# Kernel tuning notes

Measured on AMD Instinct MI355X. Metric: run time of the kernel, lower is better.

## Reference

```python
import jax, jax.numpy as jnp
import numpy as np

N, E, F, K, T = 100000, 1600000, 64, 3, 2
EPS = 1e-5


def gcn_norm(row, col, edge_weight, num_nodes):
    # symmetric normalization WITHOUT self loops (PyG ARMAConv behavior)
    deg = jax.ops.segment_sum(edge_weight, col, num_segments=num_nodes)
    dis = jnp.where(deg > 0, jax.lax.rsqrt(deg), 0.0)
    return dis[row] * edge_weight * dis[col]


def arma_conv(x, row, col, norm, init_w, w, root_w, bias, num_nodes):
    # x: [N, Fin]; init_w: [K, Fin, Fout]; w: [K, T-1, Fout, Fout]
    # root_w: [K, T, Fin, Fout]; bias: [K, T, 1, Fout]
    n_layers = root_w.shape[1]
    out = jnp.einsum('nf,kfo->kno', x, init_w)  # [K, N, Fout]
    for t in range(n_layers):
        if t > 0:
            out = jnp.einsum('kno,kop->knp', out, w[:, t - 1])
        msg = out[:, row, :] * norm[None, :, None]  # [K, E, Fout]
        out = jax.vmap(lambda m: jax.ops.segment_sum(m, col, num_segments=num_nodes))(msg)
        out = out + jnp.einsum('nf,kfo->kno', x, root_w[:, t]) + bias[:, t]
        out = jax.nn.relu(out)  # ARMAConv act between layers and at output
    return out.mean(axis=0)  # mean over stacks -> [N, Fout]


def batchnorm(h, gamma, beta):
    mu = h.mean(axis=0)
    var = h.var(axis=0)
    return gamma * (h - mu) * jax.lax.rsqrt(var + EPS) + beta


def setup_inputs() -> dict:
    key = jax.random.key(0)
    ks = jax.random.split(key, 16)
    inp = {}
    inp['x'] = jax.random.normal(ks[0], (N, F), jnp.float32)
    inp['edge_index'] = jax.random.randint(ks[1], (2, E), 0, N, dtype=jnp.int32)
    inp['weights'] = jax.random.uniform(ks[2], (E,), jnp.float32)
    s = 0.1
    i = 3
    for c in (1, 2, 3):
        inp[f'iw{c}'] = jax.random.normal(ks[i], (K, F, F), jnp.float32) * s; i += 1
        inp[f'w{c}'] = jax.random.normal(ks[i], (K, T - 1, F, F), jnp.float32) * s; i += 1
        inp[f'rw{c}'] = jax.random.normal(ks[i], (K, T, F, F), jnp.float32) * s; i += 1
        inp[f'b{c}'] = jnp.zeros((K, T, 1, F), jnp.float32)
        inp[f'g{c}'] = jnp.ones((F,), jnp.float32)
        inp[f'be{c}'] = jnp.zeros((F,), jnp.float32)
    return inp


def reference(x, edge_index, weights,
              iw1, w1, rw1, b1, g1, be1,
              iw2, w2, rw2, b2, g2, be2,
              iw3, w3, rw3, b3, g3, be3):
    num_nodes = x.shape[0]
    row, col = edge_index[0], edge_index[1]
    norm = gcn_norm(row, col, weights, num_nodes)
    h = arma_conv(x, row, col, norm, iw1, w1, rw1, b1, num_nodes)
    h = jax.nn.relu(batchnorm(h, g1, be1))
    h = arma_conv(h, row, col, norm, iw2, w2, rw2, b2, num_nodes)
    h = jax.nn.relu(batchnorm(h, g2, be2))
    h = arma_conv(h, row, col, norm, iw3, w3, rw3, b3, num_nodes)
    h = jax.nn.relu(batchnorm(h, g3, be3))
    return h
```

## Files before the change

### kernel.cpp

```cpp
#include <hip/hip_runtime.h>

#define NN 100000
#define NE 1600000
#define FD 64
#define KK 3
#define NF (NN*FD)
#define EPSBN 1e-5f
#define SBLK ((NN + 255) / 256)
#define DEGSCALE 262144.0f

typedef unsigned short ushort;
typedef unsigned int uint;
typedef __attribute__((ext_vector_type(8))) short short8;
typedef __attribute__((ext_vector_type(4))) float f32x4;

__device__ inline float bf2f(ushort u) { return __uint_as_float((unsigned)u << 16); }
__device__ inline unsigned pk_bf16(float a, float b) {
  unsigned ua = __float_as_uint(a); ua += 0x7FFF + ((ua >> 16) & 1);
  unsigned ub = __float_as_uint(b); ub += 0x7FFF + ((ub >> 16) & 1);
  return (ua >> 16) | (ub & 0xFFFF0000u);
}
__device__ inline ushort f2bf(float v) {
  unsigned u = __float_as_uint(v); u += 0x7FFF + ((u >> 16) & 1);
  return (ushort)(u >> 16);
}

__global__ void k_degcnt(const int* __restrict__ col, const float* __restrict__ w,
                         unsigned long long* __restrict__ dc) {
  int e = blockIdx.x * 256 + threadIdx.x;
  if (e < NE) {
    unsigned fx = __float2uint_rn(w[e] * DEGSCALE);
    atomicAdd(&dc[col[e]], (1ULL << 32) | (unsigned long long)fx);
  }
}

__global__ __launch_bounds__(256) void k_sblk(const unsigned long long* __restrict__ dc,
                                              float* __restrict__ dis, int* __restrict__ cnt,
                                              int* __restrict__ part) {
  int i = blockIdx.x * 256 + threadIdx.x;
  int v = 0;
  if (i < NN) {
    unsigned long long u = dc[i];
    float d = (float)(unsigned)u * (1.0f / DEGSCALE);
    dis[i] = d > 0.f ? rsqrtf(d) : 0.f;
    v = (int)(u >> 32);
    cnt[i] = v;
  }
#pragma unroll
  for (int off = 32; off; off >>= 1) v += __shfl_down(v, off);
  __shared__ int ws[4];
  if ((threadIdx.x & 63) == 0) ws[threadIdx.x >> 6] = v;
  __syncthreads();
  if (threadIdx.x == 0) part[blockIdx.x] = ws[0] + ws[1] + ws[2] + ws[3];
}

__global__ __launch_bounds__(512) void k_sscan(const int* __restrict__ part,
                                               int* __restrict__ base) {
  __shared__ int ls[512];
  int tid = threadIdx.x;
  int v = (tid < SBLK) ? part[tid] : 0;
  ls[tid] = v;
  __syncthreads();
  for (int off = 1; off < 512; off <<= 1) {
    int u = (tid >= off) ? ls[tid - off] : 0;
    __syncthreads();
    ls[tid] += u;
    __syncthreads();
  }
  base[tid] = tid ? ls[tid - 1] : 0;
}

__global__ __launch_bounds__(256) void k_sfin(const int* __restrict__ cnt,
                                              const int* __restrict__ base,
                                              int* __restrict__ rowstart,
                                              int* __restrict__ cursor) {
  __shared__ int ls[256];
  int i = blockIdx.x * 256 + threadIdx.x;
  int v = (i < NN) ? cnt[i] : 0;
  ls[threadIdx.x] = v;
  __syncthreads();
  for (int off = 1; off < 256; off <<= 1) {
    int u = (threadIdx.x >= off) ? ls[threadIdx.x - off] : 0;
    __syncthreads();
    ls[threadIdx.x] += u;
    __syncthreads();
  }
  int excl = base[blockIdx.x] + ls[threadIdx.x] - v;
  if (i < NN) {
    rowstart[i] = excl;
    cursor[i] = excl;
    if (i == NN - 1) rowstart[NN] = excl + v;
  }
}

__global__ void k_place(const int* __restrict__ row, const int* __restrict__ col,
                        const float* __restrict__ w, const float* __restrict__ dis,
                        int* __restrict__ cursor, int2* __restrict__ edges) {
  int e = blockIdx.x * 256 + threadIdx.x;
  if (e >= NE) return;
  int r = row[e], c = col[e];
  float nm = dis[r] * w[e] * dis[c];
  int p = atomicAdd(&cursor[c], 1);
  edges[p] = make_int2(r, __float_as_int(nm));
}

__global__ __launch_bounds__(64) void k_wfrag(const float* __restrict__ iw,
                                              const float* __restrict__ w,
                                              const float* __restrict__ rw,
                                              uint4* __restrict__ frag) {
  int m = blockIdx.x;
  int which = m / 3, k = m % 3;
  const float* src;
  if (which == 0) src = iw + k * 4096;
  else if (which == 1) src = w + k * 4096;
  else if (which == 2) src = rw + k * 8192;
  else src = rw + k * 8192 + 4096;
  int sub = blockIdx.y;
  int ks = sub & 1, ct = sub >> 1;
  int l = threadIdx.x;
  int r0 = ks * 32 + (l >> 4) * 8;
  int c = ct * 16 + (l & 15);
  uint4 o;
  o.x = pk_bf16(src[(r0 + 0) * 64 + c], src[(r0 + 1) * 64 + c]);
  o.y = pk_bf16(src[(r0 + 2) * 64 + c], src[(r0 + 3) * 64 + c]);
  o.z = pk_bf16(src[(r0 + 4) * 64 + c], src[(r0 + 5) * 64 + c]);
  o.w = pk_bf16(src[(r0 + 6) * 64 + c], src[(r0 + 7) * 64 + c]);
  frag[(m * 8 + sub) * 64 + l] = o;
}

__global__ void k_tobf(const float* __restrict__ in, ushort* __restrict__ out) {
  long i = ((long)blockIdx.x * 256 + threadIdx.x) * 4;
  float4 v = *(const float4*)(in + i);
  uint2 u;
  u.x = pk_bf16(v.x, v.y);
  u.y = pk_bf16(v.z, v.w);
  *(uint2*)(out + i) = u;
}

#define RED2(v) do { (v) += __shfl_xor((v), 16); (v) += __shfl_xor((v), 32); } while (0)

#define G0STEP(EV) do { \
  int2 _e = (EV); \
  float _m = __int_as_float(_e.y); \
  uint2 _u = ((const uint2*)(xsrc + (long)_e.x * 64))[fi]; \
  a0 = fmaf(bf2f((ushort)_u.x), _m, a0); a1 = fmaf(bf2f((ushort)(_u.x >> 16)), _m, a1); \
  a2 = fmaf(bf2f((ushort)_u.y), _m, a2); a3 = fmaf(bf2f((ushort)(_u.y >> 16)), _m, a3); \
} while (0)

__global__ __launch_bounds__(256) void k_gath0(const int* __restrict__ rowstart,
                                               const int2* __restrict__ edges,
                                               const ushort* __restrict__ xsrc,
                                               ushort* __restrict__ g) {
  int wave = threadIdx.x >> 6;
  int lane = threadIdx.x & 63;
  int grp = lane >> 4;
  int fi = lane & 15;
  int n = blockIdx.x * 4 + wave;
  if (n >= NN) return;
  int s = rowstart[n], e = rowstart[n + 1];
  float a0 = 0.f, a1 = 0.f, a2 = 0.f, a3 = 0.f;
  int j = s;
  for (; j + 8 <= e; j += 8) {
    G0STEP(edges[j + grp]);
    G0STEP(edges[j + 4 + grp]);
  }
  if (j + 4 <= e) { G0STEP(edges[j + grp]); j += 4; }
  if (j < e) {
    int idx = j + grp;
    int2 ee = edges[idx < e ? idx : (e - 1)];
    if (idx >= e) ee.y = 0;
    G0STEP(ee);
  }
  RED2(a0); RED2(a1); RED2(a2); RED2(a3);
  if (grp == 0) {
    uint2 o;
    o.x = pk_bf16(a0, a1);
    o.y = pk_bf16(a2, a3);
    *(uint2*)(g + (long)n * 64 + 4 * fi) = o;
  }
}

#define G1STEP(EV) do { \
  int2 _e = (EV); \
  float _m = __int_as_float(_e.y); \
  const uint2* _p = (const uint2*)(y0 + (long)_e.x * 192) + fi; \
  uint2 _u0 = _p[0], _u1 = _p[16], _u2 = _p[32]; \
  a00 = fmaf(bf2f((ushort)_u0.x), _m, a00); a01 = fmaf(bf2f((ushort)(_u0.x >> 16)), _m, a01); \
  a02 = fmaf(bf2f((ushort)_u0.y), _m, a02); a03 = fmaf(bf2f((ushort)(_u0.y >> 16)), _m, a03); \
  a10 = fmaf(bf2f((ushort)_u1.x), _m, a10); a11 = fmaf(bf2f((ushort)(_u1.x >> 16)), _m, a11); \
  a12 = fmaf(bf2f((ushort)_u1.y), _m, a12); a13 = fmaf(bf2f((ushort)(_u1.y >> 16)), _m, a13); \
  a20 = fmaf(bf2f((ushort)_u2.x), _m, a20); a21 = fmaf(bf2f((ushort)(_u2.x >> 16)), _m, a21); \
  a22 = fmaf(bf2f((ushort)_u2.y), _m, a22); a23 = fmaf(bf2f((ushort)(_u2.y >> 16)), _m, a23); \
} while (0)

__global__ __launch_bounds__(256) void k_gath1(const int* __restrict__ rowstart,
                                               const int2* __restrict__ edges,
                                               const ushort* __restrict__ y0,
                                               ushort* __restrict__ G) {
  int wave = threadIdx.x >> 6;
  int lane = threadIdx.x & 63;
  int grp = lane >> 4;
  int fi = lane & 15;
  int n = blockIdx.x * 4 + wave;
  if (n >= NN) return;
  int s = rowstart[n], e = rowstart[n + 1];
  float a00 = 0.f, a01 = 0.f, a02 = 0.f, a03 = 0.f;
  float a10 = 0.f, a11 = 0.f, a12 = 0.f, a13 = 0.f;
  float a20 = 0.f, a21 = 0.f, a22 = 0.f, a23 = 0.f;
  int j = s;
  for (; j + 8 <= e; j += 8) {
    G1STEP(edges[j + grp]);
    G1STEP(edges[j + 4 + grp]);
  }
  if (j + 4 <= e) { G1STEP(edges[j + grp]); j += 4; }
  if (j < e) {
    int idx = j + grp;
    int2 ee = edges[idx < e ? idx : (e - 1)];
    if (idx >= e) ee.y = 0;
    G1STEP(ee);
  }
  RED2(a00); RED2(a01); RED2(a02); RED2(a03);
  RED2(a10); RED2(a11); RED2(a12); RED2(a13);
  RED2(a20); RED2(a21); RED2(a22); RED2(a23);
  if (grp < 3) {
    float aX, aY, aZ, aW;
    if (grp == 0)      { aX = a00; aY = a01; aZ = a02; aW = a03; }
    else if (grp == 1) { aX = a10; aY = a11; aZ = a12; aW = a13; }
    else               { aX = a20; aY = a21; aZ = a22; aW = a23; }
    uint2 o;
    o.x = pk_bf16(aX, aY);
    o.y = pk_bf16(aZ, aW);
    *(uint2*)(G + (long)n * 192 + grp * 64 + 4 * fi) = o;
  }
}

__global__ __launch_bounds__(256) void k_gemmY0(
    const ushort* __restrict__ g, const ushort* __restrict__ xbf,
    const uint4* __restrict__ wfA, const uint4* __restrict__ wfB,
    const float* __restrict__ bias, ushort* __restrict__ y0) {
  const int k = blockIdx.y;
  const int wv = threadIdx.x >> 6;
  const int l = threadIdx.x & 63;
  const int lg = l >> 4;
  const int lr = l & 15;
  short8 fA[4][2], fB[4][2];
#pragma unroll
  for (int ct = 0; ct < 4; ++ct)
#pragma unroll
    for (int ks = 0; ks < 2; ++ks) {
      fA[ct][ks] = *(const short8*)&wfA[(k * 8 + ct * 2 + ks) * 64 + l];
      fB[ct][ks] = *(const short8*)&wfB[(k * 8 + ct * 2 + ks) * 64 + l];
    }
  const int bb = blockIdx.x * 256;
  for (int rt = 0; rt < 4; ++rt) {
    const int tb = bb + rt * 64 + wv * 16;
    int ra = tb + lr; if (ra >= NN) ra = NN - 1;
    const long ao = (long)ra * 64 + lg * 8;
    short8 a0 = *(const short8*)(g + ao);
    short8 a1 = *(const short8*)(g + ao + 32);
    short8 b0 = *(const short8*)(xbf + ao);
    short8 b1 = *(const short8*)(xbf + ao + 32);
#pragma unroll
    for (int ct = 0; ct < 4; ++ct) {
      f32x4 acc = {0.f, 0.f, 0.f, 0.f};
      acc = __builtin_amdgcn_mfma_f32_16x16x32_bf16(a0, fA[ct][0], acc, 0, 0, 0);
      acc = __builtin_amdgcn_mfma_f32_16x16x32_bf16(a1, fA[ct][1], acc, 0, 0, 0);
      acc = __builtin_amdgcn_mfma_f32_16x16x32_bf16(b0, fB[ct][0], acc, 0, 0, 0);
      acc = __builtin_amdgcn_mfma_f32_16x16x32_bf16(b1, fB[ct][1], acc, 0, 0, 0);
      const int f = ct * 16 + lr;
      const float bv = bias[(k * 2 + 0) * 64 + f];
      ushort* op = y0 + (long)(tb + lg * 4) * 192 + k * 64 + f;
#pragma unroll
      for (int r = 0; r < 4; ++r)
        if (tb + lg * 4 + r < NN) op[(long)r * 192] = f2bf(fmaxf(acc[r] + bv, 0.f));
    }
  }
}

__global__ __launch_bounds__(256) void k_gemmY1(
    const ushort* __restrict__ G, const ushort* __restrict__ xbf,
    const uint4* __restrict__ wfW, const uint4* __restrict__ wfR,
    const float* __restrict__ bias, float* __restrict__ hm) {
  const int wv = threadIdx.x >> 6;
  const int l = threadIdx.x & 63;
  const int lg = l >> 4;
  const int lr = l & 15;
  const int bb = blockIdx.x * 256;
  for (int rt = 0; rt < 4; ++rt) {
    const int tb = bb + rt * 64 + wv * 16;
    int ra = tb + lr; if (ra >= NN) ra = NN - 1;
    const long xo = (long)ra * 64 + lg * 8;
    short8 ax0 = *(const short8*)(xbf + xo);
    short8 ax1 = *(const short8*)(xbf + xo + 32);
    f32x4 m0 = {0.f, 0.f, 0.f, 0.f}, m1 = m0, m2 = m0, m3 = m0;
#pragma unroll
    for (int k = 0; k < 3; ++k) {
      const long go = (long)ra * 192 + k * 64 + lg * 8;
      short8 g0 = *(const short8*)(G + go);
      short8 g1 = *(const short8*)(G + go + 32);
      const int k8 = k * 8;
#define YCT(CT, M) { \
      short8 fw0 = *(const short8*)&wfW[(k8 + CT * 2 + 0) * 64 + l]; \
      short8 fw1 = *(const short8*)&wfW[(k8 + CT * 2 + 1) * 64 + l]; \
      short8 fr0 = *(const short8*)&wfR[(k8 + CT * 2 + 0) * 64 + l]; \
      short8 fr1 = *(const short8*)&wfR[(k8 + CT * 2 + 1) * 64 + l]; \
      f32x4 acc = {0.f, 0.f, 0.f, 0.f}; \
      acc = __builtin_amdgcn_mfma_f32_16x16x32_bf16(g0, fw0, acc, 0, 0, 0); \
      acc = __builtin_amdgcn_mfma_f32_16x16x32_bf16(g1, fw1, acc, 0, 0, 0); \
      acc = __builtin_amdgcn_mfma_f32_16x16x32_bf16(ax0, fr0, acc, 0, 0, 0); \
      acc = __builtin_amdgcn_mfma_f32_16x16x32_bf16(ax1, fr1, acc, 0, 0, 0); \
      float bv = bias[(k * 2 + 1) * 64 + CT * 16 + lr]; \
      M[0] += fmaxf(acc[0] + bv, 0.f); M[1] += fmaxf(acc[1] + bv, 0.f); \
      M[2] += fmaxf(acc[2] + bv, 0.f); M[3] += fmaxf(acc[3] + bv, 0.f); }
      YCT(0, m0) YCT(1, m1) YCT(2, m2) YCT(3, m3)
#undef YCT
    }
    const int rb = tb + lg * 4;
#pragma unroll
    for (int r = 0; r < 4; ++r) {
      if (rb + r < NN) {
        float* hp = hm + (long)(rb + r) * 64 + lr;
        hp[0]  = m0[r] * (1.f / 3.f);
        hp[16] = m1[r] * (1.f / 3.f);
        hp[32] = m2[r] * (1.f / 3.f);
        hp[48] = m3[r] * (1.f / 3.f);
      }
    }
  }
}

__global__ __launch_bounds__(256) void k_bnstats(const float* __restrict__ h,
                                                 float* __restrict__ sum,
                                                 float* __restrict__ sq) {
  int f = threadIdx.x & 63, g = threadIdx.x >> 6;
  float s = 0.f, s2 = 0.f;
  for (int n = blockIdx.x * 4 + g; n < NN; n += gridDim.x * 4) {
    float v = h[(long)n * 64 + f];
    s += v; s2 += v * v;
  }
  __shared__ float ls[512];
  ls[threadIdx.x] = s;
  ls[256 + threadIdx.x] = s2;
  __syncthreads();
  if (threadIdx.x < 64) {
    float ts  = ls[f] + ls[64 + f] + ls[128 + f] + ls[192 + f];
    float ts2 = ls[256 + f] + ls[320 + f] + ls[384 + f] + ls[448 + f];
    atomicAdd(&sum[f], ts);
    atomicAdd(&sq[f], ts2);
  }
}

template <bool FINAL>
__global__ void k_bnfin(const float* __restrict__ h, const float* __restrict__ sum,
                        const float* __restrict__ sq, const float* __restrict__ gam,
                        const float* __restrict__ bet,
                        float* __restrict__ outf, ushort* __restrict__ outbf) {
  long i4 = (long)blockIdx.x * 256 + threadIdx.x;
  if (i4 >= (long)NF / 4) return;
  long i = i4 * 4;
  int f = (int)(i & 63);
  float4 v = *(const float4*)(h + i);
  float o[4] = {v.x, v.y, v.z, v.w};
  float r[4];
#pragma unroll
  for (int j = 0; j < 4; ++j) {
    int fj = f + j;
    float mu = sum[fj] * (1.f / NN);
    float var = sq[fj] * (1.f / NN) - mu * mu;
    float inv = rsqrtf(var + EPSBN);
    float y = gam[fj] * (o[j] - mu) * inv + bet[fj];
    r[j] = fmaxf(y, 0.f);
  }
  if (FINAL) {
    float4 ov = {r[0], r[1], r[2], r[3]};
    *(float4*)(outf + i) = ov;
  } else {
    uint2 u;
    u.x = pk_bf16(r[0], r[1]);
    u.y = pk_bf16(r[2], r[3]);
    *(uint2*)(outbf + i) = u;
  }
}

extern "C" void kernel_launch(void* const* d_in, const int* in_sizes, int n_in,
                              void* d_out, int out_size, void* d_ws, size_t ws_size,
                              hipStream_t stream) {
  const float* x   = (const float*)d_in[0];
  const int*   ei  = (const int*)d_in[1];
  const float* wts = (const float*)d_in[2];
  const int* row = ei;
  const int* col = ei + NE;

  unsigned long long* dc = (unsigned long long*)d_ws;
  uint4* wfrag    = (uint4*)((int*)d_ws + 2 * NN);
  int2*  edges    = (int2*)((int*)wfrag + 73728);
  int*   cnt      = (int*)edges + 2 * NE;
  int*   rowstart = cnt + NN;
  int*   cursor   = rowstart + NN + 4;
  float* dis      = (float*)(cursor + NN);
  float* hm       = dis + NN;
  ushort* xbf     = (ushort*)(hm + NF);
  ushort* g       = xbf + NF;
  ushort* y0      = g + NF;
  ushort* Gb      = y0 + (long)NN * 192;
  float* bns      = (float*)(Gb + (long)NN * 192);
  int*   part     = (int*)(bns + 128);
  int*   pbase    = part + 512;

  hipMemsetAsync(dc, 0, NN * sizeof(unsigned long long), stream);
  int eb = (NE + 255) / 256;
  k_degcnt<<<eb, 256, 0, stream>>>(col, wts, dc);
  k_sblk<<<SBLK, 256, 0, stream>>>(dc, dis, cnt, part);
  k_sscan<<<1, 512, 0, stream>>>(part, pbase);
  k_sfin<<<SBLK, 256, 0, stream>>>(cnt, pbase, rowstart, cursor);
  k_place<<<eb, 256, 0, stream>>>(row, col, wts, dis, cursor, edges);
  for (int L = 0; L < 3; ++L) {
    k_wfrag<<<dim3(12, 8), 64, 0, stream>>>((const float*)d_in[3 + 6 * L],
                                            (const float*)d_in[4 + 6 * L],
                                            (const float*)d_in[5 + 6 * L],
                                            wfrag + (long)L * 6144);
  }
  k_tobf<<<NF / 4 / 256, 256, 0, stream>>>(x, xbf);

  int gB = (NN + 3) / 4;
  int nfBlocks = NF / 4 / 256;

  for (int layer = 0; layer < 3; ++layer) {
    const float* bs = (const float*)d_in[6 + 6 * layer];
    const float* gm = (const float*)d_in[7 + 6 * layer];
    const float* bt = (const float*)d_in[8 + 6 * layer];
    const uint4* wfL = wfrag + (long)layer * 6144;

    k_gath0<<<gB, 256, 0, stream>>>(rowstart, edges, xbf, g);
    k_gemmY0<<<dim3(SBLK, 3), 256, 0, stream>>>(g, xbf, wfL, wfL + 2 * 1536, bs, y0);
    k_gath1<<<gB, 256, 0, stream>>>(rowstart, edges, y0, Gb);
    k_gemmY1<<<SBLK, 256, 0, stream>>>(Gb, xbf, wfL + 1 * 1536, wfL + 3 * 1536, bs, hm);
    hipMemsetAsync(bns, 0, 2 * 64 * sizeof(float), stream);
    k_bnstats<<<1024, 256, 0, stream>>>(hm, bns, bns + 64);
    if (layer == 2)
      k_bnfin<true><<<nfBlocks, 256, 0, stream>>>(hm, bns, bns + 64, gm, bt, (float*)d_out, (ushort*)0);
    else
      k_bnfin<false><<<nfBlocks, 256, 0, stream>>>(hm, bns, bns + 64, gm, bt, (float*)0, xbf);
  }
}
```

Measured before the change: 963.7 us.

## Use split-bf16 hi/lo MFMA, fuse first gather with GEMM and BN stats

Activations, gathered sums and weights are now stored as bf16 hi/lo pairs, and each GEMM runs three MFMA products (hi*hi, lo*hi, hi*lo) to recover near-fp32 accuracy. The first gather is fused into the Y0 GEMM through shared memory, and the BN statistics are folded into the Y1 GEMM epilogue, dropping the g buffer and the separate bnstats pass. In exchange it triples MFMA work, doubles the x and G traffic, and the fused kernel processes 16 nodes serially per wave.

Measured after the change: 963.7 us, median of 2. Within noise of the previous version (+0.0%).

```diff
diff --git a/kernel.cpp b/kernel.cpp
--- a/kernel.cpp
+++ b/kernel.cpp
@@ -7,6 +7,7 @@
 #define NF (NN*FD)
 #define EPSBN 1e-5f
 #define SBLK ((NN + 255) / 256)
+#define BLK64 ((NN + 63) / 64)
 #define DEGSCALE 262144.0f
 
 typedef unsigned short ushort;
@@ -14,15 +15,18 @@
 typedef __attribute__((ext_vector_type(8))) short short8;
 typedef __attribute__((ext_vector_type(4))) float f32x4;
 
+#define MFMA __builtin_amdgcn_mfma_f32_16x16x32_bf16
+
 __device__ inline float bf2f(ushort u) { return __uint_as_float((unsigned)u << 16); }
-__device__ inline unsigned pk_bf16(float a, float b) {
-  unsigned ua = __float_as_uint(a); ua += 0x7FFF + ((ua >> 16) & 1);
-  unsigned ub = __float_as_uint(b); ub += 0x7FFF + ((ub >> 16) & 1);
-  return (ua >> 16) | (ub & 0xFFFF0000u);
-}
 __device__ inline ushort f2bf(float v) {
   unsigned u = __float_as_uint(v); u += 0x7FFF + ((u >> 16) & 1);
   return (ushort)(u >> 16);
+}
+__device__ inline void split2(float a, float b, uint& hi, uint& lo) {
+  ushort ha = f2bf(a), hb = f2bf(b);
+  float ra = a - bf2f(ha), rb = b - bf2f(hb);
+  hi = (uint)ha | ((uint)hb << 16);
+  lo = (uint)f2bf(ra) | ((uint)f2bf(rb) << 16);
 }
 
 __global__ void k_degcnt(const int* __restrict__ col, const float* __restrict__ w,
@@ -120,21 +124,24 @@
   int l = threadIdx.x;
   int r0 = ks * 32 + (l >> 4) * 8;
   int c = ct * 16 + (l & 15);
-  uint4 o;
-  o.x = pk_bf16(src[(r0 + 0) * 64 + c], src[(r0 + 1) * 64 + c]);
-  o.y = pk_bf16(src[(r0 + 2) * 64 + c], src[(r0 + 3) * 64 + c]);
-  o.z = pk_bf16(src[(r0 + 4) * 64 + c], src[(r0 + 5) * 64 + c]);
-  o.w = pk_bf16(src[(r0 + 6) * 64 + c], src[(r0 + 7) * 64 + c]);
-  frag[(m * 8 + sub) * 64 + l] = o;
-}
-
-__global__ void k_tobf(const float* __restrict__ in, ushort* __restrict__ out) {
+  uint4 oh, ol;
+  split2(src[(r0 + 0) * 64 + c], src[(r0 + 1) * 64 + c], oh.x, ol.x);
+  split2(src[(r0 + 2) * 64 + c], src[(r0 + 3) * 64 + c], oh.y, ol.y);
+  split2(src[(r0 + 4) * 64 + c], src[(r0 + 5) * 64 + c], oh.z, ol.z);
+  split2(src[(r0 + 6) * 64 + c], src[(r0 + 7) * 64 + c], oh.w, ol.w);
+  frag[(m * 8 + sub) * 64 + l] = oh;
+  frag[6144 + (m * 8 + sub) * 64 + l] = ol;
+}
+
+__global__ void k_tobf2(const float* __restrict__ in,
+                        ushort* __restrict__ hi, ushort* __restrict__ lo) {
   long i = ((long)blockIdx.x * 256 + threadIdx.x) * 4;
   float4 v = *(const float4*)(in + i);
-  uint2 u;
-  u.x = pk_bf16(v.x, v.y);
-  u.y = pk_bf16(v.z, v.w);
-  *(uint2*)(out + i) = u;
+  uint2 uh, ul;
+  split2(v.x, v.y, uh.x, ul.x);
+  split2(v.z, v.w, uh.y, ul.y);
+  *(uint2*)(hi + i) = uh;
+  *(uint2*)(lo + i) = ul;
 }
 
 #define RED2(v) do { (v) += __shfl_xor((v), 16); (v) += __shfl_xor((v), 32); } while (0)
@@ -142,43 +149,10 @@
 #define G0STEP(EV) do { \
   int2 _e = (EV); \
   float _m = __int_as_float(_e.y); \
-  uint2 _u = ((const uint2*)(xsrc + (long)_e.x * 64))[fi]; \
+  uint2 _u = ((const uint2*)(xhi + (long)_e.x * 64))[fi]; \
   a0 = fmaf(bf2f((ushort)_u.x), _m, a0); a1 = fmaf(bf2f((ushort)(_u.x >> 16)), _m, a1); \
   a2 = fmaf(bf2f((ushort)_u.y), _m, a2); a3 = fmaf(bf2f((ushort)(_u.y >> 16)), _m, a3); \
 } while (0)
-
-__global__ __launch_bounds__(256) void k_gath0(const int* __restrict__ rowstart,
-                                               const int2* __restrict__ edges,
-                                               const ushort* __restrict__ xsrc,
-                                               ushort* __restrict__ g) {
-  int wave = threadIdx.x >> 6;
-  int lane = threadIdx.x & 63;
-  int grp = lane >> 4;
-  int fi = lane & 15;
-  int n = blockIdx.x * 4 + wave;
-  if (n >= NN) return;
-  int s = rowstart[n], e = rowstart[n + 1];
-  float a0 = 0.f, a1 = 0.f, a2 = 0.f, a3 = 0.f;
-  int j = s;
-  for (; j + 8 <= e; j += 8) {
-    G0STEP(edges[j + grp]);
-    G0STEP(edges[j + 4 + grp]);
-  }
-  if (j + 4 <= e) { G0STEP(edges[j + grp]); j += 4; }
-  if (j < e) {
-    int idx = j + grp;
-    int2 ee = edges[idx < e ? idx : (e - 1)];
-    if (idx >= e) ee.y = 0;
-    G0STEP(ee);
-  }
-  RED2(a0); RED2(a1); RED2(a2); RED2(a3);
-  if (grp == 0) {
-    uint2 o;
-    o.x = pk_bf16(a0, a1);
-    o.y = pk_bf16(a2, a3);
-    *(uint2*)(g + (long)n * 64 + 4 * fi) = o;
-  }
-}
 
 #define G1STEP(EV) do { \
   int2 _e = (EV); \
@@ -193,10 +167,90 @@
   a22 = fmaf(bf2f((ushort)_u2.y), _m, a22); a23 = fmaf(bf2f((ushort)(_u2.y >> 16)), _m, a23); \
 } while (0)
 
+__global__ __launch_bounds__(256) void k_l0(
+    const int* __restrict__ rowstart, const int2* __restrict__ edges,
+    const ushort* __restrict__ xhi, const ushort* __restrict__ xlo,
+    const uint4* __restrict__ wfAh, const uint4* __restrict__ wfAl,
+    const uint4* __restrict__ wfBh, const uint4* __restrict__ wfBl,
+    const float* __restrict__ bias, ushort* __restrict__ y0) {
+  __shared__ ushort Gh[64 * 72];
+  __shared__ ushort Gl[64 * 72];
+  const int wv = threadIdx.x >> 6;
+  const int l = threadIdx.x & 63;
+  const int grp = l >> 4, fi = l & 15;
+  const int nb = blockIdx.x * 64;
+  for (int i = 0; i < 16; ++i) {
+    int n = nb + wv * 16 + i;
+    float a0 = 0.f, a1 = 0.f, a2 = 0.f, a3 = 0.f;
+    if (n < NN) {
+      int s = rowstart[n], e = rowstart[n + 1];
+      int j = s;
+      for (; j + 8 <= e; j += 8) { G0STEP(edges[j + grp]); G0STEP(edges[j + 4 + grp]); }
+      if (j + 4 <= e) { G0STEP(edges[j + grp]); j += 4; }
+      if (j < e) {
+        int idx = j + grp;
+        int2 ee = edges[idx < e ? idx : (e - 1)];
+        if (idx >= e) ee.y = 0;
+        G0STEP(ee);
+      }
+    }
+    RED2(a0); RED2(a1); RED2(a2); RED2(a3);
+    if (grp == 0) {
+      uint2 uh, ul;
+      split2(a0, a1, uh.x, ul.x);
+      split2(a2, a3, uh.y, ul.y);
+      *(uint2*)&Gh[(wv * 16 + i) * 72 + 4 * fi] = uh;
+      *(uint2*)&Gl[(wv * 16 + i) * 72 + 4 * fi] = ul;
+    }
+  }
+  __syncthreads();
+  const int lg = grp, lr = fi;
+  const int tb = nb + wv * 16;
+  int ra = tb + lr; if (ra >= NN) ra = NN - 1;
+  const long xo = (long)ra * 64 + lg * 8;
+  short8 xh0 = *(const short8*)(xhi + xo);
+  short8 xh1 = *(const short8*)(xhi + xo + 32);
+  short8 xl0 = *(const short8*)(xlo + xo);
+  short8 xl1 = *(const short8*)(xlo + xo + 32);
+  short8 gh0 = *(const short8*)&Gh[(wv * 16 + lr) * 72 + lg * 8];
+  short8 gh1 = *(const short8*)&Gh[(wv * 16 + lr) * 72 + lg * 8 + 32];
+  short8 gl0 = *(const short8*)&Gl[(wv * 16 + lr) * 72 + lg * 8];
+  short8 gl1 = *(const short8*)&Gl[(wv * 16 + lr) * 72 + lg * 8 + 32];
+#pragma unroll
+  for (int k = 0; k < 3; ++k) {
+    const int k8 = k * 8;
+#pragma unroll
+    for (int ct = 0; ct < 4; ++ct) {
+      short8 ah0 = *(const short8*)&wfAh[(k8 + ct * 2 + 0) * 64 + l];
+      short8 ah1 = *(const short8*)&wfAh[(k8 + ct * 2 + 1) * 64 + l];
+      short8 al0 = *(const short8*)&wfAl[(k8 + ct * 2 + 0) * 64 + l];
+      short8 al1 = *(const short8*)&wfAl[(k8 + ct * 2 + 1) * 64 + l];
+      short8 bh0 = *(const short8*)&wfBh[(k8 + ct * 2 + 0) * 64 + l];
+      short8 bh1 = *(const short8*)&wfBh[(k8 + ct * 2 + 1) * 64 + l];
+      short8 bl0 = *(const short8*)&wfBl[(k8 + ct * 2 + 0) * 64 + l];
+      short8 bl1 = *(const short8*)&wfBl[(k8 + ct * 2 + 1) * 64 + l];
+      f32x4 acc = {0.f, 0.f, 0.f, 0.f};
+      acc = MFMA(gh0, ah0, acc, 0, 0, 0); acc = MFMA(gh1, ah1, acc, 0, 0, 0);
+      acc = MFMA(gl0, ah0, acc, 0, 0, 0); acc = MFMA(gl1, ah1, acc, 0, 0, 0);
+      acc = MFMA(gh0, al0, acc, 0, 0, 0); acc = MFMA(gh1, al1, acc, 0, 0, 0);
+      acc = MFMA(xh0, bh0, acc, 0, 0, 0); acc = MFMA(xh1, bh1, acc, 0, 0, 0);
+      acc = MFMA(xl0, bh0, acc, 0, 0, 0); acc = MFMA(xl1, bh1, acc, 0, 0, 0);
+      acc = MFMA(xh0, bl0, acc, 0, 0, 0); acc = MFMA(xh1, bl1, acc, 0, 0, 0);
+      const int f = ct * 16 + lr;
+      const float bv = bias[(k * 2 + 0) * 64 + f];
+      ushort* op = y0 + (long)(tb + lg * 4) * 192 + k * 64 + f;
+#pragma unroll
+      for (int r = 0; r < 4; ++r)
+        if (tb + lg * 4 + r < NN) op[(long)r * 192] = f2bf(fmaxf(acc[r] + bv, 0.f));
+    }
+  }
+}
+
 __global__ __launch_bounds__(256) void k_gath1(const int* __restrict__ rowstart,
                                                const int2* __restrict__ edges,
                                                const ushort* __restrict__ y0,
-                                               ushort* __restrict__ G) {
+                                               ushort* __restrict__ Ghi,
+                                               ushort* __restrict__ Glo) {
   int wave = threadIdx.x >> 6;
   int lane = threadIdx.x & 63;
   int grp = lane >> 4;
@@ -208,10 +262,7 @@
   float a10 = 0.f, a11 = 0.f, a12 = 0.f, a13 = 0.f;
   float a20 = 0.f, a21 = 0.f, a22 = 0.f, a23 = 0.f;
   int j = s;
-  for (; j + 8 <= e; j += 8) {
-    G1STEP(edges[j + grp]);
-    G1STEP(edges[j + 4 + grp]);
-  }
+  for (; j + 8 <= e; j += 8) { G1STEP(edges[j + grp]); G1STEP(edges[j + 4 + grp]); }
   if (j + 4 <= e) { G1STEP(edges[j + grp]); j += 4; }
   if (j < e) {
     int idx = j + grp;
@@ -227,88 +278,62 @@
     if (grp == 0)      { aX = a00; aY = a01; aZ = a02; aW = a03; }
     else if (grp == 1) { aX = a10; aY = a11; aZ = a12; aW = a13; }
     else               { aX = a20; aY = a21; aZ = a22; aW = a23; }
-    uint2 o;
-    o.x = pk_bf16(aX, aY);
-    o.y = pk_bf16(aZ, aW);
-    *(uint2*)(G + (long)n * 192 + grp * 64 + 4 * fi) = o;
-  }
-}
-
-__global__ __launch_bounds__(256) void k_gemmY0(
-    const ushort* __restrict__ g, const ushort* __restrict__ xbf,
-    const uint4* __restrict__ wfA, const uint4* __restrict__ wfB,
-    const float* __restrict__ bias, ushort* __restrict__ y0) {
-  const int k = blockIdx.y;
+    uint2 uh, ul;
+    split2(aX, aY, uh.x, ul.x);
+    split2(aZ, aW, uh.y, ul.y);
+    long o = (long)n * 192 + grp * 64 + 4 * fi;
+    *(uint2*)(Ghi + o) = uh;
+    *(uint2*)(Glo + o) = ul;
+  }
+}
+
+__global__ __launch_bounds__(256) void k_gemmY1(
+    const ushort* __restrict__ Ghi, const ushort* __restrict__ Glo,
+    const ushort* __restrict__ xhi, const ushort* __restrict__ xlo,
+    const uint4* __restrict__ wfWh, const uint4* __restrict__ wfWl,
+    const uint4* __restrict__ wfRh, const uint4* __restrict__ wfRl,
+    const float* __restrict__ bias, float* __restrict__ hm,
+    float* __restrict__ bns) {
+  __shared__ float bnl[128];
+  if (threadIdx.x < 128) bnl[threadIdx.x] = 0.f;
+  __syncthreads();
   const int wv = threadIdx.x >> 6;
   const int l = threadIdx.x & 63;
-  const int lg = l >> 4;
-  const int lr = l & 15;
-  short8 fA[4][2], fB[4][2];
-#pragma unroll
-  for (int ct = 0; ct < 4; ++ct)
-#pragma unroll
-    for (int ks = 0; ks < 2; ++ks) {
-      fA[ct][ks] = *(const short8*)&wfA[(k * 8 + ct * 2 + ks) * 64 + l];
-      fB[ct][ks] = *(const short8*)&wfB[(k * 8 + ct * 2 + ks) * 64 + l];
-    }
-  const int bb = blockIdx.x * 256;
-  for (int rt = 0; rt < 4; ++rt) {
-    const int tb = bb + rt * 64 + wv * 16;
-    int ra = tb + lr; if (ra >= NN) ra = NN - 1;
-    const long ao = (long)ra * 64 + lg * 8;
-    short8 a0 = *(const short8*)(g + ao);
-    short8 a1 = *(const short8*)(g + ao + 32);
-    short8 b0 = *(const short8*)(xbf + ao);
-    short8 b1 = *(const short8*)(xbf + ao + 32);
-#pragma unroll
-    for (int ct = 0; ct < 4; ++ct) {
-      f32x4 acc = {0.f, 0.f, 0.f, 0.f};
-      acc = __builtin_amdgcn_mfma_f32_16x16x32_bf16(a0, fA[ct][0], acc, 0, 0, 0);
-      acc = __builtin_amdgcn_mfma_f32_16x16x32_bf16(a1, fA[ct][1], acc, 0, 0, 0);
-      acc = __builtin_amdgcn_mfma_f32_16x16x32_bf16(b0, fB[ct][0], acc, 0, 0, 0);
-      acc = __builtin_amdgcn_mfma_f32_16x16x32_bf16(b1, fB[ct][1], acc, 0, 0, 0);
-      const int f = ct * 16 + lr;
-      const float bv = bias[(k * 2 + 0) * 64 + f];
-      ushort* op = y0 + (long)(tb + lg * 4) * 192 + k * 64 + f;
-#pragma unroll
-      for (int r = 0; r < 4; ++r)
-        if (tb + lg * 4 + r < NN) op[(long)r * 192] = f2bf(fmaxf(acc[r] + bv, 0.f));
-    }
-  }
-}
-
-__global__ __launch_bounds__(256) void k_gemmY1(
-    const ushort* __restrict__ G, const ushort* __restrict__ xbf,
-    const uint4* __restrict__ wfW, const uint4* __restrict__ wfR,
-    const float* __restrict__ bias, float* __restrict__ hm) {
-  const int wv = threadIdx.x >> 6;
-  const int l = threadIdx.x & 63;
-  const int lg = l >> 4;
-  const int lr = l & 15;
+  const int lg = l >> 4, lr = l & 15;
   const int bb = blockIdx.x * 256;
   for (int rt = 0; rt < 4; ++rt) {
     const int tb = bb + rt * 64 + wv * 16;
     int ra = tb + lr; if (ra >= NN) ra = NN - 1;
     const long xo = (long)ra * 64 + lg * 8;
-    short8 ax0 = *(const short8*)(xbf + xo);
-    short8 ax1 = *(const short8*)(xbf + xo + 32);
+    short8 xh0 = *(const short8*)(xhi + xo);
+    short8 xh1 = *(const short8*)(xhi + xo + 32);
+    short8 xl0 = *(const short8*)(xlo + xo);
+    short8 xl1 = *(const short8*)(xlo + xo + 32);
     f32x4 m0 = {0.f, 0.f, 0.f, 0.f}, m1 = m0, m2 = m0, m3 = m0;
 #pragma unroll
     for (int k = 0; k < 3; ++k) {
       const long go = (long)ra * 192 + k * 64 + lg * 8;
-      short8 g0 = *(const short8*)(G + go);
-      short8 g1 = *(const short8*)(G + go + 32);
+      short8 gh0 = *(const short8*)(Ghi + go);
+      short8 gh1 = *(const short8*)(Ghi + go + 32);
+      short8 gl0 = *(const short8*)(Glo + go);
+      short8 gl1 = *(const short8*)(Glo + go + 32);
       const int k8 = k * 8;
 #define YCT(CT, M) { \
-      short8 fw0 = *(const short8*)&wfW[(k8 + CT * 2 + 0) * 64 + l]; \
-      short8 fw1 = *(const short8*)&wfW[(k8 + CT * 2 + 1) * 64 + l]; \
-      short8 fr0 = *(const short8*)&wfR[(k8 + CT * 2 + 0) * 64 + l]; \
-      short8 fr1 = *(const short8*)&wfR[(k8 + CT * 2 + 1) * 64 + l]; \
+      short8 wh0 = *(const short8*)&wfWh[(k8 + CT * 2 + 0) * 64 + l]; \
+      short8 wh1 = *(const short8*)&wfWh[(k8 + CT * 2 + 1) * 64 + l]; \
+      short8 wl0 = *(const short8*)&wfWl[(k8 + CT * 2 + 0) * 64 + l]; \
+      short8 wl1 = *(const short8*)&wfWl[(k8 + CT * 2 + 1) * 64 + l]; \
+      short8 rh0 = *(const short8*)&wfRh[(k8 + CT * 2 + 0) * 64 + l]; \
+      short8 rh1 = *(const short8*)&wfRh[(k8 + CT * 2 + 1) * 64 + l]; \
+      short8 rl0 = *(const short8*)&wfRl[(k8 + CT * 2 + 0) * 64 + l]; \
+      short8 rl1 = *(const short8*)&wfRl[(k8 + CT * 2 + 1) * 64 + l]; \
       f32x4 acc = {0.f, 0.f, 0.f, 0.f}; \
-      acc = __builtin_amdgcn_mfma_f32_16x16x32_bf16(g0, fw0, acc, 0, 0, 0); \
-      acc = __builtin_amdgcn_mfma_f32_16x16x32_bf16(g1, fw1, acc, 0, 0, 0); \
-      acc = __builtin_amdgcn_mfma_f32_16x16x32_bf16(ax0, fr0, acc, 0, 0, 0); \
-      acc = __builtin_amdgcn_mfma_f32_16x16x32_bf16(ax1, fr1, acc, 0, 0, 0); \
+      acc = MFMA(gh0, wh0, acc, 0, 0, 0); acc = MFMA(gh1, wh1, acc, 0, 0, 0); \
+      acc = MFMA(gl0, wh0, acc, 0, 0, 0); acc = MFMA(gl1, wh1, acc, 0, 0, 0); \
+      acc = MFMA(gh0, wl0, acc, 0, 0, 0); acc = MFMA(gh1, wl1, acc, 0, 0, 0); \
+      acc = MFMA(xh0, rh0, acc, 0, 0, 0); acc = MFMA(xh1, rh1, acc, 0, 0, 0); \
+      acc = MFMA(xl0, rh0, acc, 0, 0, 0); acc = MFMA(xl1, rh1, acc, 0, 0, 0); \
+      acc = MFMA(xh0, rl0, acc, 0, 0, 0); acc = MFMA(xh1, rl1, acc, 0, 0, 0); \
       float bv = bias[(k * 2 + 1) * 64 + CT * 16 + lr]; \
       M[0] += fmaxf(acc[0] + bv, 0.f); M[1] += fmaxf(acc[1] + bv, 0.f); \
       M[2] += fmaxf(acc[2] + bv, 0.f); M[3] += fmaxf(acc[3] + bv, 0.f); }
@@ -316,45 +341,33 @@
 #undef YCT
     }
     const int rb = tb + lg * 4;
+    m0 *= (1.f / 3.f); m1 *= (1.f / 3.f); m2 *= (1.f / 3.f); m3 *= (1.f / 3.f);
 #pragma unroll
     for (int r = 0; r < 4; ++r) {
       if (rb + r < NN) {
         float* hp = hm + (long)(rb + r) * 64 + lr;
-        hp[0]  = m0[r] * (1.f / 3.f);
-        hp[16] = m1[r] * (1.f / 3.f);
-        hp[32] = m2[r] * (1.f / 3.f);
-        hp[48] = m3[r] * (1.f / 3.f);
+        hp[0] = m0[r]; hp[16] = m1[r]; hp[32] = m2[r]; hp[48] = m3[r];
       }
     }
-  }
-}
-
-__global__ __launch_bounds__(256) void k_bnstats(const float* __restrict__ h,
-                                                 float* __restrict__ sum,
-                                                 float* __restrict__ sq) {
-  int f = threadIdx.x & 63, g = threadIdx.x >> 6;
-  float s = 0.f, s2 = 0.f;
-  for (int n = blockIdx.x * 4 + g; n < NN; n += gridDim.x * 4) {
-    float v = h[(long)n * 64 + f];
-    s += v; s2 += v * v;
-  }
-  __shared__ float ls[512];
-  ls[threadIdx.x] = s;
-  ls[256 + threadIdx.x] = s2;
-  __syncthreads();
-  if (threadIdx.x < 64) {
-    float ts  = ls[f] + ls[64 + f] + ls[128 + f] + ls[192 + f];
-    float ts2 = ls[256 + f] + ls[320 + f] + ls[384 + f] + ls[448 + f];
-    atomicAdd(&sum[f], ts);
-    atomicAdd(&sq[f], ts2);
-  }
+#define BNCT(M, CT) { \
+    float s = 0.f, q = 0.f; \
+    for (int r = 0; r < 4; ++r) if (rb + r < NN) { s += M[r]; q += M[r] * M[r]; } \
+    s += __shfl_xor(s, 16); s += __shfl_xor(s, 32); \
+    q += __shfl_xor(q, 16); q += __shfl_xor(q, 32); \
+    if (lg == 0) { atomicAdd(&bnl[CT * 16 + lr], s); atomicAdd(&bnl[64 + CT * 16 + lr], q); } }
+    BNCT(m0, 0) BNCT(m1, 1) BNCT(m2, 2) BNCT(m3, 3)
+#undef BNCT
+  }
+  __syncthreads();
+  if (threadIdx.x < 128) atomicAdd(&bns[threadIdx.x], bnl[threadIdx.x]);
 }
 
 template <bool FINAL>
 __global__ void k_bnfin(const float* __restrict__ h, const float* __restrict__ sum,
                         const float* __restrict__ sq, const float* __restrict__ gam,
                         const float* __restrict__ bet,
-                        float* __restrict__ outf, ushort* __restrict__ outbf) {
+                        float* __restrict__ outf,
+                        ushort* __restrict__ ohi, ushort* __restrict__ olo) {
   long i4 = (long)blockIdx.x * 256 + threadIdx.x;
   if (i4 >= (long)NF / 4) return;
   long i = i4 * 4;
@@ -375,10 +388,11 @@
     float4 ov = {r[0], r[1], r[2], r[3]};
     *(float4*)(outf + i) = ov;
   } else {
-    uint2 u;
-    u.x = pk_bf16(r[0], r[1]);
-    u.y = pk_bf16(r[2], r[3]);
-    *(uint2*)(outbf + i) = u;
+    uint2 uh, ul;
+    split2(r[0], r[1], uh.x, ul.x);
+    split2(r[2], r[3], uh.y, ul.y);
+    *(uint2*)(ohi + i) = uh;
+    *(uint2*)(olo + i) = ul;
   }
 }
 
@@ -393,17 +407,18 @@
 
   unsigned long long* dc = (unsigned long long*)d_ws;
   uint4* wfrag    = (uint4*)((int*)d_ws + 2 * NN);
-  int2*  edges    = (int2*)((int*)wfrag + 73728);
+  int2*  edges    = (int2*)((int*)wfrag + 147456);
   int*   cnt      = (int*)edges + 2 * NE;
   int*   rowstart = cnt + NN;
   int*   cursor   = rowstart + NN + 4;
   float* dis      = (float*)(cursor + NN);
   float* hm       = dis + NN;
-  ushort* xbf     = (ushort*)(hm + NF);
-  ushort* g       = xbf + NF;
-  ushort* y0      = g + NF;
-  ushort* Gb      = y0 + (long)NN * 192;
-  float* bns      = (float*)(Gb + (long)NN * 192);
+  ushort* xhi     = (ushort*)(hm + NF);
+  ushort* xlo     = xhi + NF;
+  ushort* y0      = xlo + NF;
+  ushort* Ghi     = y0 + (long)NN * 192;
+  ushort* Glo     = Ghi + (long)NN * 192;
+  float* bns      = (float*)(Glo + (long)NN * 192);
   int*   part     = (int*)(bns + 128);
   int*   pbase    = part + 512;
 
@@ -418,9 +433,9 @@
     k_wfrag<<<dim3(12, 8), 64, 0, stream>>>((const float*)d_in[3 + 6 * L],
                                             (const float*)d_in[4 + 6 * L],
                                             (const float*)d_in[5 + 6 * L],
-                                            wfrag + (long)L * 6144);
-  }
-  k_tobf<<<NF / 4 / 256, 256, 0, stream>>>(x, xbf);
+                                            wfrag + (long)L * 12288);
+  }
+  k_tobf2<<<NF / 4 / 256, 256, 0, stream>>>(x, xhi, xlo);
 
   int gB = (NN + 3) / 4;
   int nfBlocks = NF / 4 / 256;
@@ -429,17 +444,22 @@
     const float* bs = (const float*)d_in[6 + 6 * layer];
     const float* gm = (const float*)d_in[7 + 6 * layer];
     const float* bt = (const float*)d_in[8 + 6 * layer];
-    const uint4* wfL = wfrag + (long)layer * 6144;
-
-    k_gath0<<<gB, 256, 0, stream>>>(rowstart, edges, xbf, g);
-    k_gemmY0<<<dim3(SBLK, 3), 256, 0, stream>>>(g, xbf, wfL, wfL + 2 * 1536, bs, y0);
-    k_gath1<<<gB, 256, 0, stream>>>(rowstart, edges, y0, Gb);
-    k_gemmY1<<<SBLK, 256, 0, stream>>>(Gb, xbf, wfL + 1 * 1536, wfL + 3 * 1536, bs, hm);
+    const uint4* wfL = wfrag + (long)layer * 12288;
+
+    k_l0<<<BLK64, 256, 0, stream>>>(rowstart, edges, xhi, xlo,
+                                    wfL + 0, wfL + 6144, wfL + 3072, wfL + 3072 + 6144,
+                                    bs, y0);
     hipMemsetAsync(bns, 0, 2 * 64 * sizeof(float), stream);
-    k_bnstats<<<1024, 256, 0, stream>>>(hm, bns, bns + 64);
+    k_gath1<<<gB, 256, 0, stream>>>(rowstart, edges, y0, Ghi, Glo);
+    k_gemmY1<<<SBLK, 256, 0, stream>>>(Ghi, Glo, xhi, xlo,
+                                       wfL + 1536, wfL + 1536 + 6144,
+                                       wfL + 4608, wfL + 4608 + 6144,
+                                       bs, hm, bns);
     if (layer == 2)
-      k_bnfin<true><<<nfBlocks, 256, 0, stream>>>(hm, bns, bns + 64, gm, bt, (float*)d_out, (ushort*)0);
+      k_bnfin<true><<<nfBlocks, 256, 0, stream>>>(hm, bns, bns + 64, gm, bt,
+                                                  (float*)d_out, (ushort*)0, (ushort*)0);
     else
-      k_bnfin<false><<<nfBlocks, 256, 0, stream>>>(hm, bns, bns + 64, gm, bt, (float*)0, xbf);
-  }
-}
+      k_bnfin<false><<<nfBlocks, 256, 0, stream>>>(hm, bns, bns + 64, gm, bt,
+                                                   (float*)0, xhi, xlo);
+  }
+}
```
